# Optimization experiments

Measured on AMD Instinct MI355X. Metric: run time of the kernel, lower is better.

Reference implementation:

```python
import jax, jax.numpy as jnp
import numpy as np

VOCAB = 8192
CTX = 4  # sum(context_length) = sum((2,2))
BATCH = 1024


def setup_inputs() -> dict:
    key = jax.random.key(0)
    k1, k2, k3 = jax.random.split(key, 3)
    contexts = jax.random.randint(k1, (BATCH, CTX), 0, VOCAB, dtype=jnp.int64 if jax.config.read('jax_enable_x64') else jnp.int32)
    # torch Linear(in=CTX*VOCAB, out=VOCAB): weight [VOCAB, CTX*VOCAB], bias [VOCAB]
    fc_w = jax.random.normal(k2, (VOCAB, CTX * VOCAB), dtype=jnp.float32) * 0.02
    fc_b = jax.random.normal(k3, (VOCAB,), dtype=jnp.float32) * 0.02
    return {"contexts": contexts, "fc_w": fc_w, "fc_b": fc_b}


def reference(contexts, fc_w, fc_b):
    # out[b, o] = sum_{i,v} onehot(contexts)[b,i,v] * fc_w[o, i*V + v] + fc_b[o]
    #           = sum_i fc_w[o, i*V + contexts[b,i]] + fc_b[o]
    # i.e. the dense one-hot GEMM is a row-gather over the fc weight.
    V = fc_b.shape[0]
    B, C = contexts.shape
    # [C, V_in, V_out]
    w = fc_w.reshape(V, C, V).transpose(1, 2, 0)
    pos = jnp.arange(C)[None, :]          # [1, C]
    gathered = w[pos, contexts]           # [B, C, V_out]
    return gathered.sum(axis=1) + fc_b    # [B, V_out]
```

## Files before the change

kernel.cpp:

```cpp
#include <hip/hip_runtime.h>

#define VOCAB 8192
#define CTX 4
#define BATCH 1024
#define OBLK 16
#define NCHUNK (OBLK * CTX)

__global__ __launch_bounds__(1024) void cbow_kernel(
    const int*   __restrict__ contexts,
    const float* __restrict__ fc_w,
    const float* __restrict__ fc_b,
    float*       __restrict__ out)
{
    __shared__ float lds[2][VOCAB];

    const int t  = threadIdx.x;
    const int o0 = blockIdx.x * OBLK;
    const size_t base = (size_t)o0 * (CTX * VOCAB);

    const int4 cv = ((const int4*)contexts)[t];
    const int cc[4] = {cv.x, cv.y, cv.z, cv.w};

    float acc[OBLK];
#pragma unroll
    for (int j = 0; j < OBLK; ++j) acc[j] = fc_b[o0 + j];

    {
        const float4* s0 = (const float4*)(fc_w + base);
        float4 a = s0[t];
        float4 b = s0[1024 + t];
        float4* dst = (float4*)lds[0];
        dst[t]        = a;
        dst[1024 + t] = b;
    }
    const float4* s1 = (const float4*)(fc_w + base + VOCAB);
    float4 ra = s1[t];
    float4 rb = s1[1024 + t];
    asm volatile("s_waitcnt lgkmcnt(0)\n\ts_barrier" ::: "memory");

#pragma unroll
    for (int k = 0; k < NCHUNK; ++k) {
        float4 na, nb;
        if (k + 2 < NCHUNK) {
            const float4* src = (const float4*)(fc_w + base + (size_t)(k + 2) * VOCAB);
            na = src[t];
            nb = src[1024 + t];
        }

        if (k + 1 < NCHUNK) {
            float4* dst = (float4*)lds[(k + 1) & 1];
            dst[t]        = ra;
            dst[1024 + t] = rb;
        }

        acc[k >> 2] += lds[k & 1][cc[k & 3]];

        ra = na;
        rb = nb;

        if (k < NCHUNK - 1)
            asm volatile("s_waitcnt lgkmcnt(0)\n\ts_barrier" ::: "memory");
    }

    float4* op = (float4*)(out + (size_t)t * VOCAB + o0);
#pragma unroll
    for (int j = 0; j < OBLK / 4; ++j) {
        float4 v;
        v.x = acc[4 * j + 0];
        v.y = acc[4 * j + 1];
        v.z = acc[4 * j + 2];
        v.w = acc[4 * j + 3];
        op[j] = v;
    }
}

extern "C" void kernel_launch(void* const* d_in, const int* in_sizes, int n_in,
                              void* d_out, int out_size, void* d_ws, size_t ws_size,
                              hipStream_t stream) {
    const int*   contexts = (const int*)d_in[0];
    const float* fc_w     = (const float*)d_in[1];
    const float* fc_b     = (const float*)d_in[2];
    float*       out      = (float*)d_out;

    dim3 grid(VOCAB / OBLK);
    dim3 block(1024);
    cbow_kernel<<<grid, block, 0, stream>>>(contexts, fc_w, fc_b, out);
}
```

Measured before the change: 201.6 us.

## Deepen weight prefetch pipeline to a 4-slot LDS ring and double output block

Each block now handles 32 output rows instead of 16, and the LDS buffer becomes a 4-slot ring. Global loads are issued four chunks ahead, and LDS writes happen two chunks ahead, so more memory latency can hide behind the barrier-separated gather steps. The cost is more registers and LDS per block (128KB LDS, 32 accumulators plus extra prefetch float4s) and half as many blocks (256), which may lower occupancy and parallelism across CUs.

```diff
diff --git a/kernel.cpp b/kernel.cpp
--- a/kernel.cpp
+++ b/kernel.cpp
@@ -3,8 +3,9 @@
 #define VOCAB 8192
 #define CTX 4
 #define BATCH 1024
-#define OBLK 16
+#define OBLK 32
 #define NCHUNK (OBLK * CTX)
+#define RING 4
 
 __global__ __launch_bounds__(1024) void cbow_kernel(
     const int*   __restrict__ contexts,
@@ -12,7 +13,7 @@
     const float* __restrict__ fc_b,
     float*       __restrict__ out)
 {
-    __shared__ float lds[2][VOCAB];
+    __shared__ float lds[RING][VOCAB];
 
     const int t  = threadIdx.x;
     const int o0 = blockIdx.x * OBLK;
@@ -25,38 +26,42 @@
 #pragma unroll
     for (int j = 0; j < OBLK; ++j) acc[j] = fc_b[o0 + j];
 
-    {
-        const float4* s0 = (const float4*)(fc_w + base);
-        float4 a = s0[t];
-        float4 b = s0[1024 + t];
-        float4* dst = (float4*)lds[0];
+#pragma unroll
+    for (int k = 0; k < 2; ++k) {
+        const float4* src = (const float4*)(fc_w + base + (size_t)k * VOCAB);
+        float4 a = src[t];
+        float4 b = src[1024 + t];
+        float4* dst = (float4*)lds[k];
         dst[t]        = a;
         dst[1024 + t] = b;
     }
-    const float4* s1 = (const float4*)(fc_w + base + VOCAB);
-    float4 ra = s1[t];
-    float4 rb = s1[1024 + t];
+    const float4* s2 = (const float4*)(fc_w + base + (size_t)2 * VOCAB);
+    float4 pa = s2[t];
+    float4 pb = s2[1024 + t];
+    const float4* s3 = (const float4*)(fc_w + base + (size_t)3 * VOCAB);
+    float4 na = s3[t];
+    float4 nb = s3[1024 + t];
     asm volatile("s_waitcnt lgkmcnt(0)\n\ts_barrier" ::: "memory");
 
 #pragma unroll
     for (int k = 0; k < NCHUNK; ++k) {
-        float4 na, nb;
-        if (k + 2 < NCHUNK) {
-            const float4* src = (const float4*)(fc_w + base + (size_t)(k + 2) * VOCAB);
-            na = src[t];
-            nb = src[1024 + t];
+        float4 fa, fb;
+        if (k + 4 < NCHUNK) {
+            const float4* src = (const float4*)(fc_w + base + (size_t)(k + 4) * VOCAB);
+            fa = src[t];
+            fb = src[1024 + t];
         }
 
-        if (k + 1 < NCHUNK) {
-            float4* dst = (float4*)lds[(k + 1) & 1];
-            dst[t]        = ra;
-            dst[1024 + t] = rb;
+        if (k + 2 < NCHUNK) {
+            float4* dst = (float4*)lds[(k + 2) & (RING - 1)];
+            dst[t]        = pa;
+            dst[1024 + t] = pb;
         }
 
-        acc[k >> 2] += lds[k & 1][cc[k & 3]];
+        acc[k >> 2] += lds[k & (RING - 1)][cc[k & 3]];
 
-        ra = na;
-        rb = nb;
+        pa = na; pb = nb;
+        na = fa; nb = fb;
 
         if (k < NCHUNK - 1)
             asm volatile("s_waitcnt lgkmcnt(0)\n\ts_barrier" ::: "memory");
```

Result: slower. 213.6 us (+6.0%).
